# Kernel optimization log

Hardware: AMD Instinct MI355X
Metric: run time of the kernel (lower is better)

## Reference

```python
import jax, jax.numpy as jnp
import numpy as np

B, IN, H, OUT, BS = 2048, 1024, 2048, 1024, 32
RB = H // BS   # 64 block rows of fc2
CB = H // BS   # 64 block cols of fc2
DENSITY = 0.5
K = int(CB * DENSITY)  # 32 nonzero block-cols per block row
NNZ = RB * K           # 2048 nonzero blocks


def setup_inputs() -> dict:
    key = jax.random.key(0)
    k0, k1, k2, k3, k4, k5, k6 = jax.random.split(key, 7)
    # Fixed BSR sparsity structure (constant indices), built with numpy
    rng = np.random.default_rng(0)
    cols = np.stack([np.sort(rng.choice(CB, size=K, replace=False)) for _ in range(RB)])
    col_indices = jnp.asarray(cols.reshape(-1), dtype=jnp.int32)          # [NNZ]
    crow_indices = jnp.asarray(np.arange(RB + 1) * K, dtype=jnp.int32)    # [RB+1]
    s = 0.02
    return {
        "x": jax.random.normal(k0, (B, IN), jnp.float32),
        "W1": jax.random.normal(k1, (H, IN), jnp.float32) * s,
        "b1": jax.random.normal(k2, (H,), jnp.float32) * s,
        "crow_indices": crow_indices,
        "col_indices": col_indices,
        "values": jax.random.normal(k3, (NNZ, BS, BS), jnp.float32) * s,  # BSR blocks of fc2.weight [H,H]
        "b2": jax.random.normal(k4, (H,), jnp.float32) * s,
        "W3": jax.random.normal(k5, (OUT, H), jnp.float32) * s,
        "b3": jax.random.normal(k6, (OUT,), jnp.float32) * s,
    }


def bsr_linear(h, crow_indices, col_indices, values, bias):
    # y = h @ W.T + bias, W stored as BSR (block rows = out blocks, block cols = in blocks)
    b = h.shape[0]
    nnz, bs, _ = values.shape
    rb = crow_indices.shape[0] - 1
    hb = h.reshape(b, -1, bs)                      # [B, CB, bs]
    hg = hb[:, col_indices]                        # [B, NNZ, bs] gather input blocks per nnz block
    # contribution of block k (row r, col c): x_block[c] @ values[k].T
    contrib = jnp.einsum("bnj,nij->nbi", hg, values)  # [NNZ, B, bs]
    # block-row id of each nnz block, jit-safe via searchsorted on crow
    row_ids = jnp.searchsorted(crow_indices, jnp.arange(nnz, dtype=crow_indices.dtype), side="right") - 1
    yb = jax.ops.segment_sum(contrib, row_ids, num_segments=rb)  # [RB, B, bs]
    return jnp.transpose(yb, (1, 0, 2)).reshape(b, rb * bs) + bias


def reference(x, W1, b1, crow_indices, col_indices, values, b2, W3, b3):
    x = x.reshape(x.shape[0], -1)                 # Flatten
    h = jax.nn.relu(x @ W1.T + b1)                # fc1 + ReLU
    h = jax.nn.relu(bsr_linear(h, crow_indices, col_indices, values, b2))  # BSR fc2 + ReLU
    return h @ W3.T + b3                          # fc3
```

## Files before the change

kernel.cpp:

```cpp
#include <hip/hip_runtime.h>
#include <hip/hip_bf16.h>


typedef __attribute__((ext_vector_type(8))) short bf16x8;
typedef __attribute__((ext_vector_type(4))) float f32x4;

__device__ __forceinline__ unsigned short f2bf(float f) {
    union { float f; unsigned int u; } c; c.f = f;
    unsigned int u = c.u;
    u += 0x7fffu + ((u >> 16) & 1u);
    return (unsigned short)(u >> 16);
}

__device__ __forceinline__ void async16(const void* g, void* l) {
    __builtin_amdgcn_global_load_lds(
        (const __attribute__((address_space(1))) void*)g,
        (__attribute__((address_space(3))) void*)l,
        16, 0, 0);
}

template<int N>
__device__ __forceinline__ void vm_wait() {
    asm volatile("s_waitcnt vmcnt(%0)" :: "n"(N) : "memory");
}
__device__ __forceinline__ void barrier() {
    asm volatile("" ::: "memory");
    __builtin_amdgcn_s_barrier();
    asm volatile("" ::: "memory");
}

__global__ __launch_bounds__(256) void cvt4(
    const float* __restrict__ x,  const float* __restrict__ w1,
    const float* __restrict__ w3, const float* __restrict__ v,
    unsigned short* __restrict__ xb,  unsigned short* __restrict__ w1b,
    unsigned short* __restrict__ w3b, unsigned short* __restrict__ vb)
{
    const int NE = 1 << 21;
    int e = (blockIdx.x * 256 + threadIdx.x) * 4;
    int a = e >> 21;
    int off = e & (NE - 1);
    const float* src = (a == 0) ? x : (a == 1) ? w1 : (a == 2) ? w3 : v;
    unsigned short* dst = (a == 0) ? xb : (a == 1) ? w1b : (a == 2) ? w3b : vb;
    float4 vv = *reinterpret_cast<const float4*>(src + off);
    ushort4 o;
    o.x = f2bf(vv.x); o.y = f2bf(vv.y); o.z = f2bf(vv.z); o.w = f2bf(vv.w);
    *reinterpret_cast<ushort4*>(dst + off) = o;
}

__global__ __launch_bounds__(256) void combine2(
    const float* __restrict__ p0, const float* __restrict__ p1,
    const float* __restrict__ b3, float* __restrict__ out)
{
    int i = (blockIdx.x * 256 + threadIdx.x) * 4;
    float4 a = *reinterpret_cast<const float4*>(p0 + i);
    float4 b = *reinterpret_cast<const float4*>(p1 + i);
    float4 c = *reinterpret_cast<const float4*>(b3 + (i & 1023));
    float4 o = {a.x + b.x + c.x, a.y + b.y + c.y,
                a.z + b.z + c.z, a.w + b.w + c.w};
    *reinterpret_cast<float4*>(out + i) = o;
}

template<int BM, int BN, int MCL, int KSPLIT, int RELU, int OUTMODE>
__global__ __launch_bounds__(256) void gemm_bt(
    const unsigned short* __restrict__ A,
    const unsigned short* __restrict__ B,
    const float* __restrict__ bias,
    void* __restrict__ C0,
    void* __restrict__ C1,
    int M, int N, int K)
{
    constexpr int BK = 64;
    constexpr int MR = BM / 32;
    constexpr int NR = BN / 32;
    constexpr int AI = BM / 32;
    constexpr int BI = BN / 32;
    constexpr int LPS = AI + BI;
    __shared__ unsigned short As[3][BM * BK];
    __shared__ unsigned short Bs[3][BN * BK];

    const int t = threadIdx.x;
    const int w = t >> 6;
    const int l = t & 63;

    const int id = blockIdx.x;
    const int xcd = id & 7;
    int j = id >> 3;
    int ks = 0;
    if (KSPLIT == 2) { ks = j & 1; j >>= 1; }
    const int mt = xcd * MCL + (j & (MCL - 1));
    const int nt = j / MCL;
    const int bm = mt * BM;
    const int bn = nt * BN;
    const int kb = ks * (K / KSPLIT);

    const int wm = (w >> 1) * (BM / 2);
    const int wn = (w & 1) * (BN / 2);

    f32x4 acc[MR][NR];
    #pragma unroll
    for (int i = 0; i < MR; ++i)
        #pragma unroll
        for (int jj = 0; jj < NR; ++jj)
            acc[i][jj] = (f32x4){0.f, 0.f, 0.f, 0.f};

    const int arow = bm + w * (BM / 4) + (l >> 3);
    const int brow = bn + w * (BN / 4) + (l >> 3);
    const int scol = ((l & 7) ^ (l >> 3)) * 8;

    const int fr = l & 15;
    const int kg = l >> 4;
    const int fq = l >> 4;

    auto stage = [&](int buf, int kt) {
        const int k0 = kb + kt * BK;
        #pragma unroll
        for (int i = 0; i < AI; ++i)
            async16(A + (size_t)(arow + i * 8) * K + k0 + scol,
                    &As[buf][(w * (BM / 4) + i * 8) * BK]);
        #pragma unroll
        for (int i = 0; i < BI; ++i)
            async16(B + (size_t)(brow + i * 8) * K + k0 + scol,
                    &Bs[buf][(w * (BN / 4) + i * 8) * BK]);
    };

    auto compute = [&](int buf) {
        #pragma unroll
        for (int kk = 0; kk < 2; ++kk) {
            const int pc = ((kk * 4 + kg) ^ (fr & 7)) * 8;
            bf16x8 af[MR], bg[NR];
            #pragma unroll
            for (int i = 0; i < MR; ++i)
                af[i] = *reinterpret_cast<const bf16x8*>(
                    &As[buf][(wm + i * 16 + fr) * BK + pc]);
            #pragma unroll
            for (int jj = 0; jj < NR; ++jj)
                bg[jj] = *reinterpret_cast<const bf16x8*>(
                    &Bs[buf][(wn + jj * 16 + fr) * BK + pc]);
            #pragma unroll
            for (int i = 0; i < MR; ++i)
                #pragma unroll
                for (int jj = 0; jj < NR; ++jj)
                    acc[i][jj] = __builtin_amdgcn_mfma_f32_16x16x32_bf16(
                        af[i], bg[jj], acc[i][jj], 0, 0, 0);
        }
    };

    const int nK = (K / KSPLIT) >> 6;
    stage(0, 0);
    stage(1, 1);
    int cur = 0;
    int nxt = 2;
    for (int kt = 0; kt < nK; ++kt) {
        if (kt + 1 < nK) vm_wait<LPS>();
        else             vm_wait<0>();
        barrier();
        if (kt + 2 < nK) stage(nxt, kt + 2);
        compute(cur);
        cur = (cur == 2) ? 0 : cur + 1;
        nxt = (nxt == 2) ? 0 : nxt + 1;
    }

    #pragma unroll
    for (int i = 0; i < MR; ++i) {
        const int row0 = bm + wm + i * 16 + fq * 4;
        #pragma unroll
        for (int jj = 0; jj < NR; ++jj) {
            const int col = bn + wn + jj * 16 + fr;
            const float bv = (OUTMODE == 2) ? 0.f : bias[col];
            #pragma unroll
            for (int v = 0; v < 4; ++v) {
                float r = acc[i][jj][v] + bv;
                if (RELU) r = fmaxf(r, 0.f);
                const size_t off = (size_t)(row0 + v) * N + col;
                if (OUTMODE == 1)
                    ((unsigned short*)C0)[off] = f2bf(r);
                else
                    ((float*)(ks ? C1 : C0))[off] = r;
            }
        }
    }
}

__global__ __launch_bounds__(256) void bsr_layer(
    const unsigned short* __restrict__ h,
    const int* __restrict__ crow,
    const int* __restrict__ cols,
    const unsigned short* __restrict__ vals,
    const float* __restrict__ b2,
    unsigned short* __restrict__ h2)
{
    __shared__ unsigned short Hs[2][128 * 64];
    __shared__ unsigned short Vs[2][32 * 64];
    __shared__ int colsS[64];
    const int t = threadIdx.x;
    const int w = t >> 6;
    const int l = t & 63;

    const int id = blockIdx.x;
    const int xcd = id & 7;
    const int j2 = id >> 3;
    const int bt = xcd * 2 + (j2 & 1);
    const int r  = j2 >> 1;
    const int bm = bt * 128;

    const int s = crow[r];
    const int cnt = crow[r + 1] - s;
    const int wrow = w * 32;

    if (t < cnt) colsS[t] = cols[s + t];

    f32x4 acc[2][2];
    #pragma unroll
    for (int i = 0; i < 2; ++i)
        #pragma unroll
        for (int jj = 0; jj < 2; ++jj)
            acc[i][jj] = (f32x4){0.f, 0.f, 0.f, 0.f};

    const int fr = l & 15;
    const int kg = l >> 4;
    const int lr = l >> 3;
    const int sc = (l & 7) ^ lr;

    auto stage = [&](int buf, int js) {
        const int n0 = s + 2 * js;
        const bool tail = (2 * js + 1 >= cnt);
        const int c0 = colsS[2 * js];
        const int c1 = tail ? c0 : colsS[2 * js + 1];
        const int n1 = tail ? n0 : n0 + 1;
        #pragma unroll
        for (int i = 0; i < 4; ++i) {
            const int row = bm + w * 32 + i * 8 + lr;
            const int col = (sc & 4) ? c1 * 32 + (sc & 3) * 8 : c0 * 32 + sc * 8;
            async16(h + (size_t)row * 2048 + col,
                    &Hs[buf][(w * 32 + i * 8) * 64]);
        }
        const int vrow = w * 8 + lr;
        if (!tail || !(sc & 4)) {
            const unsigned short* src =
                vals + (size_t)((sc & 4) ? n1 : n0) * 1024 + vrow * 32 + (sc & 3) * 8;
            async16(src, &Vs[buf][(w * 8) * 64]);
        } else {
            bf16x8 z = (bf16x8){0,0,0,0,0,0,0,0};
            *reinterpret_cast<bf16x8*>(&Vs[buf][vrow * 64 + (l & 7) * 8]) = z;
        }
    };

    auto compute = [&](int buf) {
        #pragma unroll
        for (int kk = 0; kk < 2; ++kk) {
            const int pc = ((kk * 4 + kg) ^ (fr & 7)) * 8;
            bf16x8 af[2], bg[2];
            #pragma unroll
            for (int i = 0; i < 2; ++i)
                af[i] = *reinterpret_cast<const bf16x8*>(
                    &Hs[buf][(wrow + i * 16 + fr) * 64 + pc]);
            #pragma unroll
            for (int jj = 0; jj < 2; ++jj)
                bg[jj] = *reinterpret_cast<const bf16x8*>(
                    &Vs[buf][(jj * 16 + fr) * 64 + pc]);
            #pragma unroll
            for (int i = 0; i < 2; ++i)
                #pragma unroll
                for (int jj = 0; jj < 2; ++jj)
                    acc[i][jj] = __builtin_amdgcn_mfma_f32_16x16x32_bf16(
                        af[i], bg[jj], acc[i][jj], 0, 0, 0);
        }
    };

    __syncthreads();
    const int nsteps = (cnt + 1) >> 1;
    stage(0, 0);
    if (nsteps > 1) stage(1, 1);
    int cur = 0;
    for (int js = 0; js < nsteps - 1; ++js) {
        vm_wait<5>();
        barrier();
        compute(cur);
        barrier();
        if (js + 2 < nsteps) stage(cur, js + 2);
        cur ^= 1;
    }
    vm_wait<0>();
    barrier();
    compute(cur);

    const int fq = l >> 4;
    #pragma unroll
    for (int i = 0; i < 2; ++i) {
        const int row0 = bm + wrow + i * 16 + fq * 4;
        #pragma unroll
        for (int jj = 0; jj < 2; ++jj) {
            const int col = r * 32 + jj * 16 + fr;
            const float bv = b2[col];
            #pragma unroll
            for (int v = 0; v < 4; ++v) {
                float rv = fmaxf(acc[i][jj][v] + bv, 0.f);
                h2[(size_t)(row0 + v) * 2048 + col] = f2bf(rv);
            }
        }
    }
}

extern "C" void kernel_launch(void* const* d_in, const int* in_sizes, int n_in,
                              void* d_out, int out_size, void* d_ws, size_t ws_size,
                              hipStream_t stream) {
    const float* x    = (const float*)d_in[0];
    const float* W1   = (const float*)d_in[1];
    const float* b1   = (const float*)d_in[2];
    const int*   crow = (const int*)d_in[3];
    const int*   cols = (const int*)d_in[4];
    const float* vals = (const float*)d_in[5];
    const float* b2   = (const float*)d_in[6];
    const float* W3   = (const float*)d_in[7];
    const float* b3   = (const float*)d_in[8];
    float* out = (float*)d_out;

    const int NE = 2 * 1024 * 1024;
    unsigned short* xb  = (unsigned short*)d_ws;
    unsigned short* w1b = xb  + NE;
    unsigned short* w3b = w1b + NE;
    unsigned short* vb  = w3b + NE;
    unsigned short* hb  = vb  + NE;
    unsigned short* h2b = hb  + 2 * NE;
    float* p0 = (float*)d_ws;
    float* p1 = (float*)hb;

    cvt4<<<8192, 256, 0, stream>>>(x, W1, W3, vals, xb, w1b, w3b, vb);

    gemm_bt<128, 64, 2, 1, 1, 1><<<512, 256, 0, stream>>>(
        xb, w1b, b1, hb, nullptr, 2048, 2048, 1024);
    bsr_layer<<<1024, 256, 0, stream>>>(hb, crow, cols, vb, b2, h2b);
    gemm_bt<64, 64, 4, 2, 0, 2><<<1024, 256, 0, stream>>>(
        h2b, w3b, nullptr, p0, p1, 2048, 1024, 2048);
    combine2<<<2048, 256, 0, stream>>>(p0, p1, b3, out);

    (void)in_sizes; (void)n_in; (void)out_size; (void)ws_size;
}
```

Measured before the change: 86.52 us.

## Use 128x128 tiles with 8 waves and 3-deep prefetch in dense GEMMs

```diff
diff --git a/kernel.cpp b/kernel.cpp
--- a/kernel.cpp
+++ b/kernel.cpp
@@ -60,8 +60,8 @@
     *reinterpret_cast<float4*>(out + i) = o;
 }
 
-template<int BM, int BN, int MCL, int KSPLIT, int RELU, int OUTMODE>
-__global__ __launch_bounds__(256) void gemm_bt(
+template<int MCL, int KSPLIT, int RELU, int OUTMODE>
+__global__ __launch_bounds__(512) void gemm8(
     const unsigned short* __restrict__ A,
     const unsigned short* __restrict__ B,
     const float* __restrict__ bias,
@@ -69,12 +69,8 @@
     void* __restrict__ C1,
     int M, int N, int K)
 {
-    constexpr int BK = 64;
-    constexpr int MR = BM / 32;
-    constexpr int NR = BN / 32;
-    constexpr int AI = BM / 32;
-    constexpr int BI = BN / 32;
-    constexpr int LPS = AI + BI;
+    constexpr int BM = 128, BN = 128, BK = 64;
+    constexpr int LPS = 4;
     __shared__ unsigned short As[3][BM * BK];
     __shared__ unsigned short Bs[3][BN * BK];
 
@@ -93,19 +89,18 @@
     const int bn = nt * BN;
     const int kb = ks * (K / KSPLIT);
 
-    const int wm = (w >> 1) * (BM / 2);
-    const int wn = (w & 1) * (BN / 2);
-
-    f32x4 acc[MR][NR];
+    const int wm = (w >> 2) * 64;
+    const int wn = (w & 3) * 32;
+
+    f32x4 acc[4][2];
     #pragma unroll
-    for (int i = 0; i < MR; ++i)
-        #pragma unroll
-        for (int jj = 0; jj < NR; ++jj)
+    for (int i = 0; i < 4; ++i)
+        #pragma unroll
+        for (int jj = 0; jj < 2; ++jj)
             acc[i][jj] = (f32x4){0.f, 0.f, 0.f, 0.f};
 
-    const int arow = bm + w * (BM / 4) + (l >> 3);
-    const int brow = bn + w * (BN / 4) + (l >> 3);
-    const int scol = ((l & 7) ^ (l >> 3)) * 8;
+    const int r8 = l >> 3;
+    const int scol = ((l & 7) ^ r8) * 8;
 
     const int fr = l & 15;
     const int kg = l >> 4;
@@ -114,32 +109,32 @@
     auto stage = [&](int buf, int kt) {
         const int k0 = kb + kt * BK;
         #pragma unroll
-        for (int i = 0; i < AI; ++i)
-            async16(A + (size_t)(arow + i * 8) * K + k0 + scol,
-                    &As[buf][(w * (BM / 4) + i * 8) * BK]);
-        #pragma unroll
-        for (int i = 0; i < BI; ++i)
-            async16(B + (size_t)(brow + i * 8) * K + k0 + scol,
-                    &Bs[buf][(w * (BN / 4) + i * 8) * BK]);
+        for (int i = 0; i < 2; ++i)
+            async16(A + (size_t)(bm + i * 64 + w * 8 + r8) * K + k0 + scol,
+                    &As[buf][(i * 64 + w * 8) * BK]);
+        #pragma unroll
+        for (int i = 0; i < 2; ++i)
+            async16(B + (size_t)(bn + i * 64 + w * 8 + r8) * K + k0 + scol,
+                    &Bs[buf][(i * 64 + w * 8) * BK]);
     };
 
     auto compute = [&](int buf) {
         #pragma unroll
         for (int kk = 0; kk < 2; ++kk) {
             const int pc = ((kk * 4 + kg) ^ (fr & 7)) * 8;
-            bf16x8 af[MR], bg[NR];
-            #pragma unroll
-            for (int i = 0; i < MR; ++i)
+            bf16x8 af[4], bg[2];
+            #pragma unroll
+            for (int i = 0; i < 4; ++i)
                 af[i] = *reinterpret_cast<const bf16x8*>(
                     &As[buf][(wm + i * 16 + fr) * BK + pc]);
             #pragma unroll
-            for (int jj = 0; jj < NR; ++jj)
+            for (int jj = 0; jj < 2; ++jj)
                 bg[jj] = *reinterpret_cast<const bf16x8*>(
                     &Bs[buf][(wn + jj * 16 + fr) * BK + pc]);
             #pragma unroll
-            for (int i = 0; i < MR; ++i)
+            for (int i = 0; i < 4; ++i)
                 #pragma unroll
-                for (int jj = 0; jj < NR; ++jj)
+                for (int jj = 0; jj < 2; ++jj)
                     acc[i][jj] = __builtin_amdgcn_mfma_f32_16x16x32_bf16(
                         af[i], bg[jj], acc[i][jj], 0, 0, 0);
         }
@@ -148,23 +143,28 @@
     const int nK = (K / KSPLIT) >> 6;
     stage(0, 0);
     stage(1, 1);
+    stage(2, 2);
     int cur = 0;
-    int nxt = 2;
     for (int kt = 0; kt < nK; ++kt) {
-        if (kt + 1 < nK) vm_wait<LPS>();
-        else             vm_wait<0>();
+        if (kt < nK - 2)       vm_wait<2 * LPS>();
+        else if (kt == nK - 2) vm_wait<LPS>();
+        else                   vm_wait<0>();
         barrier();
-        if (kt + 2 < nK) stage(nxt, kt + 2);
         compute(cur);
+        if (kt + 3 < nK) {
+            barrier();
+            stage(cur, kt + 3);
+        } else if (kt + 1 < nK) {
+            barrier();
+        }
         cur = (cur == 2) ? 0 : cur + 1;
-        nxt = (nxt == 2) ? 0 : nxt + 1;
     }
 
     #pragma unroll
-    for (int i = 0; i < MR; ++i) {
+    for (int i = 0; i < 4; ++i) {
         const int row0 = bm + wm + i * 16 + fq * 4;
         #pragma unroll
-        for (int jj = 0; jj < NR; ++jj) {
+        for (int jj = 0; jj < 2; ++jj) {
             const int col = bn + wn + jj * 16 + fr;
             const float bv = (OUTMODE == 2) ? 0.f : bias[col];
             #pragma unroll
@@ -327,10 +327,10 @@
 
     cvt4<<<8192, 256, 0, stream>>>(x, W1, W3, vals, xb, w1b, w3b, vb);
 
-    gemm_bt<128, 64, 2, 1, 1, 1><<<512, 256, 0, stream>>>(
+    gemm8<2, 1, 1, 1><<<256, 512, 0, stream>>>(
         xb, w1b, b1, hb, nullptr, 2048, 2048, 1024);
     bsr_layer<<<1024, 256, 0, stream>>>(hb, crow, cols, vb, b2, h2b);
-    gemm_bt<64, 64, 4, 2, 0, 2><<<1024, 256, 0, stream>>>(
+    gemm8<2, 2, 0, 2><<<256, 512, 0, stream>>>(
         h2b, w3b, nullptr, p0, p1, 2048, 1024, 2048);
     combine2<<<2048, 256, 0, stream>>>(p0, p1, b3, out);
 
```

After: 82.79 us. 1.05x faster.
